# Optimization experiments

Hardware: AMD Instinct MI355X
Metric: run time of the kernel (lower is better)

## Reference

```python
import jax, jax.numpy as jnp
import numpy as np

S, N, E, H = 4096, 32, 512, 8
DK = E // H


def setup_inputs() -> dict:
    key = jax.random.key(0)
    ks = jax.random.split(key, 6)
    w = lambda k, shp: (jax.random.normal(k, shp, dtype=jnp.float32) * 0.02)
    return {
        "src": jax.random.normal(ks[0], (S, N, E), dtype=jnp.float32),
        "Wq": w(ks[1], (E, E)), "bq": jnp.zeros((E,), jnp.float32),
        "Wk": w(ks[2], (E, E)), "bk": jnp.zeros((E,), jnp.float32),
        "Wv": w(ks[3], (E, E)), "bv": jnp.zeros((E,), jnp.float32),
        "Wo": w(ks[4], (E, E)), "bo": jnp.zeros((E,), jnp.float32),
        "Wl": w(ks[5], (E, E)), "bl": jnp.zeros((E,), jnp.float32),
    }


def reference(src, Wq, bq, Wk, bk, Wv, bv, Wo, bo, Wl, bl):
    # src: (S, N, E). encoder_norm=False, pos=None, dropout inactive (eval).
    s, n, e = src.shape
    h, dk = H, DK
    l = s // 2  # single middle query -> L == 1 decode-style branch
    # projections (torch Linear: x @ W.T + b)
    k = (src @ Wk.T + bk).reshape(s, n, h, dk)          # (S,N,h,dk)
    v = (src @ Wv.T + bv).reshape(s, n, h, dk)          # (S,N,h,dk)
    q = (src[l] @ Wq.T + bq).reshape(n, h, dk)          # (N,h,dk)
    # scores: (q*k).sum over dk, scaled -> (N,h,S)
    scores = jnp.einsum('nhd,snhd->nhs', q, k) / (dk ** 0.5)
    attn = jax.nn.softmax(scores, axis=-1)              # (N,h,S)
    out = jnp.einsum('nhs,snhd->nhd', attn, v).reshape(n, e)  # (N,E)
    out = out @ Wo.T + bo                               # MHA output linear
    out = out @ Wl.T + bl                               # layer's final linear
    return out[None]  # (1, N, E)
```

## Files before the change

kernel.cpp:

```cpp
#include <hip/hip_runtime.h>

#define SS 4096
#define NB 32
#define EE 512
#define HH 8
#define DKK 64
#define LQ 2048
#define NCHUNK 16

#define DPPADD(dst, src, ctrl)                                              \
  dst += __int_as_float(__builtin_amdgcn_update_dpp(                        \
      0, __float_as_int(src), ctrl, 0xF, 0xF, true))

__global__ __launch_bounds__(256) void k_qproj(const float* __restrict__ src,
                                               const float* __restrict__ Wq,
                                               const float* __restrict__ bq,
                                               const float* __restrict__ Wk,
                                               float* __restrict__ qk) {
  __shared__ float qd[DKK];
  int n = blockIdx.x >> 3, h = blockIdx.x & 7;
  int tid = threadIdx.x;
  int d = tid >> 2, part = tid & 3;
  const float4* xs = (const float4*)(src + ((size_t)LQ * NB + n) * EE);
  const float4* wr = (const float4*)(Wq + (size_t)(h * DKK + d) * EE);
  float acc = 0.f;
#pragma unroll 8
  for (int i = 0; i < 32; ++i) {
    float4 a = xs[part * 32 + i], b = wr[part * 32 + i];
    acc = fmaf(a.x, b.x, fmaf(a.y, b.y, fmaf(a.z, b.z, fmaf(a.w, b.w, acc))));
  }
  DPPADD(acc, acc, 0xB1);
  DPPADD(acc, acc, 0x4E);
  if (part == 0) qd[d] = acc + bq[h * DKK + d];
  __syncthreads();
  float a0 = 0.f, a1 = 0.f;
#pragma unroll 8
  for (int d2 = 0; d2 < DKK; ++d2) {
    float qv = qd[d2];
    const float* row = Wk + (size_t)(h * DKK + d2) * EE;
    a0 = fmaf(qv, row[tid], a0);
    a1 = fmaf(qv, row[tid + 256], a1);
  }
  size_t base = (size_t)(n * HH + h) * EE;
  qk[base + tid] = a0;
  qk[base + tid + 256] = a1;
}

__global__ __launch_bounds__(256, 2) void k_fused(const float* __restrict__ src,
                                                  const float* __restrict__ qk,
                                                  float* __restrict__ part,
                                                  float* __restrict__ lw) {
  __shared__ float4 cb4[4][HH * EE / 4];
  __shared__ float lbuf[4 * HH];
  int b = blockIdx.x;
  int n = b >> 4, c = b & 15;
  int tid = threadIdx.x, wave = tid >> 6, lane = tid & 63;

  const int SLOT[8] = {0, 1, 2, 3, 7, 6, 5, 4};
  const float4* qk4 = (const float4*)qk;
  float4 qf[16];
#pragma unroll
  for (int j = 0; j < HH; ++j) {
    int hj = (lane & 7) ^ SLOT[j];
    int qbase = (n * HH + hj) * (EE / 4);
    qf[2 * j] = qk4[qbase + lane];
    qf[2 * j + 1] = qk4[qbase + 64 + lane];
  }

  float4 acc[16];
#pragma unroll
  for (int i = 0; i < 16; ++i) acc[i] = make_float4(0.f, 0.f, 0.f, 0.f);
  float lp = 0.f;

  const size_t rowstep = (size_t)NB * (EE / 4);
  const float4* sp = (const float4*)src +
                     ((size_t)((c << 8) + wave * 2) * NB + n) * (EE / 4);
  float4 cA0 = sp[lane], cA1 = sp[64 + lane];
  float4 cB0 = sp[rowstep + lane], cB1 = sp[rowstep + 64 + lane];
  sp += 8 * rowstep;
  float4 nA0 = sp[lane], nA1 = sp[64 + lane];
  float4 nB0 = sp[rowstep + lane], nB1 = sp[rowstep + 64 + lane];

#pragma unroll 2
  for (int it = 0; it < 32; ++it) {
    float4 aA = cA0, dA = cA1, aB = cB0, dB = cB1;
    cA0 = nA0; cA1 = nA1; cB0 = nB0; cB1 = nB1;
    if (it < 30) {
      sp += 8 * rowstep;
      nA0 = sp[lane]; nA1 = sp[64 + lane];
      nB0 = sp[rowstep + lane]; nB1 = sp[rowstep + 64 + lane];
    }
    float pA[8], pB[8];
#pragma unroll
    for (int j = 0; j < HH; ++j) {
      float4 u = qf[2 * j], v = qf[2 * j + 1];
      pA[j] = fmaf(aA.x, u.x, fmaf(aA.y, u.y, fmaf(aA.z, u.z, fmaf(aA.w, u.w,
              fmaf(dA.x, v.x, fmaf(dA.y, v.y, fmaf(dA.z, v.z, dA.w * v.w)))))));
      pB[j] = fmaf(aB.x, u.x, fmaf(aB.y, u.y, fmaf(aB.z, u.z, fmaf(aB.w, u.w,
              fmaf(dB.x, v.x, fmaf(dB.y, v.y, fmaf(dB.z, v.z, dB.w * v.w)))))));
    }
    DPPADD(pA[0], pA[1], 0xB1);  DPPADD(pB[0], pB[1], 0xB1);
    DPPADD(pA[2], pA[3], 0xB1);  DPPADD(pB[2], pB[3], 0xB1);
    DPPADD(pA[4], pA[5], 0xB1);  DPPADD(pB[4], pB[5], 0xB1);
    DPPADD(pA[6], pA[7], 0xB1);  DPPADD(pB[6], pB[7], 0xB1);
    DPPADD(pA[0], pA[2], 0x4E);  DPPADD(pB[0], pB[2], 0x4E);
    DPPADD(pA[4], pA[6], 0x4E);  DPPADD(pB[4], pB[6], 0x4E);
    DPPADD(pA[0], pA[4], 0x141); DPPADD(pB[0], pB[4], 0x141);
    DPPADD(pA[0], pA[0], 0x128); DPPADD(pB[0], pB[0], 0x128);
    pA[0] += __shfl_xor(pA[0], 16, 64);
    pB[0] += __shfl_xor(pB[0], 16, 64);
    pA[0] += __shfl_xor(pA[0], 32, 64);
    pB[0] += __shfl_xor(pB[0], 32, 64);
    float eA = __expf(pA[0] * 0.125f);
    float eB = __expf(pB[0] * 0.125f);
    lp += eA + eB;
    float wA[8], wB[8];
#pragma unroll
    for (int h = 0; h < HH; ++h) {
      wA[h] = __uint_as_float(__builtin_amdgcn_readlane(__float_as_uint(eA), h));
      wB[h] = __uint_as_float(__builtin_amdgcn_readlane(__float_as_uint(eB), h));
    }
#pragma unroll
    for (int h = 0; h < HH; ++h) {
      float w1 = wA[h], w2 = wB[h];
      acc[2 * h].x = fmaf(w1, aA.x, acc[2 * h].x);
      acc[2 * h].y = fmaf(w1, aA.y, acc[2 * h].y);
      acc[2 * h].z = fmaf(w1, aA.z, acc[2 * h].z);
      acc[2 * h].w = fmaf(w1, aA.w, acc[2 * h].w);
      acc[2 * h + 1].x = fmaf(w1, dA.x, acc[2 * h + 1].x);
      acc[2 * h + 1].y = fmaf(w1, dA.y, acc[2 * h + 1].y);
      acc[2 * h + 1].z = fmaf(w1, dA.z, acc[2 * h + 1].z);
      acc[2 * h + 1].w = fmaf(w1, dA.w, acc[2 * h + 1].w);
      acc[2 * h].x = fmaf(w2, aB.x, acc[2 * h].x);
      acc[2 * h].y = fmaf(w2, aB.y, acc[2 * h].y);
      acc[2 * h].z = fmaf(w2, aB.z, acc[2 * h].z);
      acc[2 * h].w = fmaf(w2, aB.w, acc[2 * h].w);
      acc[2 * h + 1].x = fmaf(w2, dB.x, acc[2 * h + 1].x);
      acc[2 * h + 1].y = fmaf(w2, dB.y, acc[2 * h + 1].y);
      acc[2 * h + 1].z = fmaf(w2, dB.z, acc[2 * h + 1].z);
      acc[2 * h + 1].w = fmaf(w2, dB.w, acc[2 * h + 1].w);
    }
  }

#pragma unroll
  for (int h = 0; h < HH; ++h) {
    cb4[wave][h * 128 + lane] = acc[2 * h];
    cb4[wave][h * 128 + 64 + lane] = acc[2 * h + 1];
  }
  if (lane < 8) lbuf[wave * 8 + lane] = lp;
  __syncthreads();
  float4* pb4 = (float4*)(part + (size_t)b * (HH * EE));
#pragma unroll
  for (int j = 0; j < 4; ++j) {
    int idx = tid + j * 256;
    float4 s0 = cb4[0][idx], s1 = cb4[1][idx], s2 = cb4[2][idx], s3 = cb4[3][idx];
    float4 o;
    o.x = s0.x + s1.x + s2.x + s3.x;
    o.y = s0.y + s1.y + s2.y + s3.y;
    o.z = s0.z + s1.z + s2.z + s3.z;
    o.w = s0.w + s1.w + s2.w + s3.w;
    pb4[idx] = o;
  }
  if (tid < 8)
    lw[b * 8 + tid] = lbuf[tid] + lbuf[8 + tid] + lbuf[16 + tid] + lbuf[24 + tid];
}

__global__ __launch_bounds__(256) void k_ctxv(const float* __restrict__ part,
                                              const float* __restrict__ lw,
                                              const float* __restrict__ Wv,
                                              const float* __restrict__ bv,
                                              float* __restrict__ vout) {
  __shared__ float ctxs[EE];
  __shared__ float linvs;
  int n = blockIdx.x >> 3, h = blockIdx.x & 7;
  int tid = threadIdx.x, wave = tid >> 6, lane = tid & 63;
  if (tid < 16) {
    float l = lw[(n * NCHUNK + tid) * 8 + h];
    DPPADD(l, l, 0xB1);
    DPPADD(l, l, 0x4E);
    DPPADD(l, l, 0x141);
    DPPADD(l, l, 0x128);
    if (tid == 0) linvs = 1.f / l;
  }
  float s0 = 0.f, s1 = 0.f;
#pragma unroll
  for (int c2 = 0; c2 < NCHUNK; ++c2) {
    const float* pb = part + (size_t)(n * NCHUNK + c2) * 4096 + h * EE;
    s0 += pb[tid];
    s1 += pb[tid + 256];
  }
  ctxs[tid] = s0;
  ctxs[tid + 256] = s1;
  __syncthreads();
  const float4* cx = (const float4*)ctxs;
  float4 c0 = cx[lane], c1 = cx[64 + lane];
  float li = linvs;
  const float4* Wv4 = (const float4*)Wv;
#pragma unroll 4
  for (int k = 0; k < 16; ++k) {
    int r = h * 64 + wave * 16 + k;
    float4 w0 = Wv4[(size_t)r * 128 + lane], w1 = Wv4[(size_t)r * 128 + 64 + lane];
    float d = fmaf(c0.x, w0.x, fmaf(c0.y, w0.y, fmaf(c0.z, w0.z, fmaf(c0.w, w0.w,
              fmaf(c1.x, w1.x, fmaf(c1.y, w1.y, fmaf(c1.z, w1.z, c1.w * w1.w)))))));
    DPPADD(d, d, 0xB1);
    DPPADD(d, d, 0x4E);
    DPPADD(d, d, 0x141);
    DPPADD(d, d, 0x128);
    d += __shfl_xor(d, 16, 64);
    d += __shfl_xor(d, 32, 64);
    if (lane == 0) vout[(size_t)n * EE + r] = d * li + bv[r];
  }
}

__global__ __launch_bounds__(64) void k_gemv(const float* __restrict__ x,
                                             const float* __restrict__ W,
                                             const float* __restrict__ bias,
                                             float* __restrict__ y) {
  int r = blockIdx.x >> 2, g = blockIdx.x & 3;
  int lane = threadIdx.x;
  const float4* W4 = (const float4*)W;
  const float4* x4 = (const float4*)x;
  float4 w0 = W4[r * 128 + lane];
  float4 w1 = W4[r * 128 + 64 + lane];
  const int SLOT[8] = {0, 1, 2, 3, 7, 6, 5, 4};
  float acc[8];
#pragma unroll
  for (int j = 0; j < 8; ++j) {
    int n = g * 8 + ((lane & 7) ^ SLOT[j]);
    float4 a = x4[n * 128 + lane], d = x4[n * 128 + 64 + lane];
    acc[j] = fmaf(a.x, w0.x, fmaf(a.y, w0.y, fmaf(a.z, w0.z, fmaf(a.w, w0.w,
             fmaf(d.x, w1.x, fmaf(d.y, w1.y, fmaf(d.z, w1.z, d.w * w1.w)))))));
  }
  DPPADD(acc[0], acc[1], 0xB1);
  DPPADD(acc[2], acc[3], 0xB1);
  DPPADD(acc[4], acc[5], 0xB1);
  DPPADD(acc[6], acc[7], 0xB1);
  DPPADD(acc[0], acc[2], 0x4E);
  DPPADD(acc[4], acc[6], 0x4E);
  DPPADD(acc[0], acc[4], 0x141);
  DPPADD(acc[0], acc[0], 0x128);
  acc[0] += __shfl_xor(acc[0], 16, 64);
  acc[0] += __shfl_xor(acc[0], 32, 64);
  if (lane < 8) y[(size_t)(g * 8 + lane) * EE + r] = acc[0] + bias[r];
}

extern "C" void kernel_launch(void* const* d_in, const int* in_sizes, int n_in,
                              void* d_out, int out_size, void* d_ws, size_t ws_size,
                              hipStream_t stream) {
  const float* src = (const float*)d_in[0];
  const float* Wq  = (const float*)d_in[1];
  const float* bq  = (const float*)d_in[2];
  const float* Wk  = (const float*)d_in[3];
  const float* Wv  = (const float*)d_in[5];
  const float* bv  = (const float*)d_in[6];
  const float* Wo  = (const float*)d_in[7];
  const float* bo  = (const float*)d_in[8];
  const float* Wl  = (const float*)d_in[9];
  const float* bl  = (const float*)d_in[10];
  float* out = (float*)d_out;

  float* ws = (float*)d_ws;
  float* qk   = ws;
  float* lw   = qk + 131072;
  float* vout = lw + 4096;
  float* y1   = vout + 16384;
  float* part = y1 + 16384;

  k_qproj<<<256, 256, 0, stream>>>(src, Wq, bq, Wk, qk);
  k_fused<<<NB * NCHUNK, 256, 0, stream>>>(src, qk, part, lw);
  k_ctxv<<<256, 256, 0, stream>>>(part, lw, Wv, bv, vout);
  k_gemv<<<2048, 64, 0, stream>>>(vout, Wo, bo, y1);
  k_gemv<<<2048, 64, 0, stream>>>(y1, Wl, bl, out);
}
```

Measured before the change: 83.65 us.

## Stage src rows through LDS with async global_load_lds four-deep pipeline

Replaces the register double-buffered src loads in the fused attention kernel with asynchronous global-to-LDS loads (global_load_lds) into a per-wave 4-slot ring, synchronised by manual vmcnt/lgkmcnt waits. This deepens prefetch to hide HBM latency and frees the registers that held the next rows. The cross-wave reduction is reworked to reuse the staging buffer with a two-phase pairwise add, so LDS use stays roughly the same. It relies on hand-placed waitcnt counts being correct and adds extra barriers in the epilogue.

After: 85.30 us. About the same (+2.0%).

```diff
diff --git a/kernel.cpp b/kernel.cpp
--- a/kernel.cpp
+++ b/kernel.cpp
@@ -11,6 +11,18 @@
 #define DPPADD(dst, src, ctrl)                                              \
   dst += __int_as_float(__builtin_amdgcn_update_dpp(                        \
       0, __float_as_int(src), ctrl, 0xF, 0xF, true))
+
+#define VMWAIT(n) asm volatile("s_waitcnt vmcnt(" #n ")" ::: "memory")
+#define LGKMWAIT0() asm volatile("s_waitcnt lgkmcnt(0)" ::: "memory")
+
+typedef const __attribute__((address_space(1))) void gvoid_t;
+typedef __attribute__((address_space(3))) void lvoid_t;
+
+__device__ __forceinline__ void stage_row(const float* g, float* l, int lane) {
+  __builtin_amdgcn_global_load_lds((gvoid_t*)(g + lane * 4), (lvoid_t*)l, 16, 0, 0);
+  __builtin_amdgcn_global_load_lds((gvoid_t*)(g + 256 + lane * 4),
+                                   (lvoid_t*)(l + 256), 16, 0, 0);
+}
 
 __global__ __launch_bounds__(256) void k_qproj(const float* __restrict__ src,
                                                const float* __restrict__ Wq,
@@ -50,7 +62,7 @@
                                                   const float* __restrict__ qk,
                                                   float* __restrict__ part,
                                                   float* __restrict__ lw) {
-  __shared__ float4 cb4[4][HH * EE / 4];
+  __shared__ float stage[4][4][2][EE];
   __shared__ float lbuf[4 * HH];
   int b = blockIdx.x;
   int n = b >> 4, c = b & 15;
@@ -72,23 +84,29 @@
   for (int i = 0; i < 16; ++i) acc[i] = make_float4(0.f, 0.f, 0.f, 0.f);
   float lp = 0.f;
 
-  const size_t rowstep = (size_t)NB * (EE / 4);
-  const float4* sp = (const float4*)src +
-                     ((size_t)((c << 8) + wave * 2) * NB + n) * (EE / 4);
-  float4 cA0 = sp[lane], cA1 = sp[64 + lane];
-  float4 cB0 = sp[rowstep + lane], cB1 = sp[rowstep + 64 + lane];
-  sp += 8 * rowstep;
-  float4 nA0 = sp[lane], nA1 = sp[64 + lane];
-  float4 nB0 = sp[rowstep + lane], nB1 = sp[rowstep + 64 + lane];
-
-#pragma unroll 2
+  const size_t rowstep = (size_t)NB * EE;
+  const size_t step8 = 8 * rowstep;
+  const float* g0 = src + (((size_t)(c << 8) + wave * 2) * NB + n) * EE;
+#pragma unroll
+  for (int p = 0; p < 4; ++p) {
+    const float* gp = g0 + p * step8;
+    stage_row(gp, &stage[wave][p][0][0], lane);
+    stage_row(gp + rowstep, &stage[wave][p][1][0], lane);
+  }
+  const float* gs = g0 + 4 * step8;
+
   for (int it = 0; it < 32; ++it) {
-    float4 aA = cA0, dA = cA1, aB = cB0, dB = cB1;
-    cA0 = nA0; cA1 = nA1; cB0 = nB0; cB1 = nB1;
-    if (it < 30) {
-      sp += 8 * rowstep;
-      nA0 = sp[lane]; nA1 = sp[64 + lane];
-      nB0 = sp[rowstep + lane]; nB1 = sp[rowstep + 64 + lane];
+    int slot = it & 3;
+    if (it < 28) { VMWAIT(12); }
+    else if (it == 28) { VMWAIT(0); }
+    const float4* sa = (const float4*)&stage[wave][slot][0][0];
+    float4 aA = sa[lane], dA = sa[64 + lane];
+    float4 aB = sa[128 + lane], dB = sa[192 + lane];
+    if (it < 28) {
+      LGKMWAIT0();
+      stage_row(gs, &stage[wave][slot][0][0], lane);
+      stage_row(gs + rowstep, &stage[wave][slot][1][0], lane);
+      gs += step8;
     }
     float pA[8], pB[8];
 #pragma unroll
@@ -142,23 +160,43 @@
     }
   }
 
-#pragma unroll
-  for (int h = 0; h < HH; ++h) {
-    cb4[wave][h * 128 + lane] = acc[2 * h];
-    cb4[wave][h * 128 + 64 + lane] = acc[2 * h + 1];
+  __syncthreads();
+  float4* e4 = (float4*)stage;
+  if ((wave & 1) == 0) {
+    int p = wave >> 1;
+#pragma unroll
+    for (int h = 0; h < HH; ++h) {
+      e4[p * 1024 + h * 128 + lane] = acc[2 * h];
+      e4[p * 1024 + h * 128 + 64 + lane] = acc[2 * h + 1];
+    }
   }
   if (lane < 8) lbuf[wave * 8 + lane] = lp;
+  __syncthreads();
+  if (wave & 1) {
+    int p = wave >> 1;
+#pragma unroll
+    for (int h = 0; h < HH; ++h) {
+      int i0 = p * 1024 + h * 128 + lane;
+      float4 t = e4[i0];
+      t.x += acc[2 * h].x; t.y += acc[2 * h].y;
+      t.z += acc[2 * h].z; t.w += acc[2 * h].w;
+      e4[i0] = t;
+      int i1 = i0 + 64;
+      float4 u = e4[i1];
+      u.x += acc[2 * h + 1].x; u.y += acc[2 * h + 1].y;
+      u.z += acc[2 * h + 1].z; u.w += acc[2 * h + 1].w;
+      e4[i1] = u;
+    }
+  }
   __syncthreads();
   float4* pb4 = (float4*)(part + (size_t)b * (HH * EE));
 #pragma unroll
   for (int j = 0; j < 4; ++j) {
     int idx = tid + j * 256;
-    float4 s0 = cb4[0][idx], s1 = cb4[1][idx], s2 = cb4[2][idx], s3 = cb4[3][idx];
+    float4 a0 = e4[idx], a1 = e4[1024 + idx];
     float4 o;
-    o.x = s0.x + s1.x + s2.x + s3.x;
-    o.y = s0.y + s1.y + s2.y + s3.y;
-    o.z = s0.z + s1.z + s2.z + s3.z;
-    o.w = s0.w + s1.w + s2.w + s3.w;
+    o.x = a0.x + a1.x; o.y = a0.y + a1.y;
+    o.z = a0.z + a1.z; o.w = a0.w + a1.w;
     pb4[idx] = o;
   }
   if (tid < 8)
```
